# Optimization experiments

Hardware: AMD Instinct MI355X
Metric: run time of the kernel (lower is better)

## Reference

```python
import jax, jax.numpy as jnp
import numpy as np

B, S, D, H = 4, 1024, 1024, 16
HD = D // H
MAX_DIST, WIN, MAX_SPAN = 512, 256, 512
TEMP_SCALE = 0.01
EPS = 1e-5


def _ln(x, g, b):
    m = x.mean(-1, keepdims=True)
    v = ((x - m) ** 2).mean(-1, keepdims=True)
    return (x - m) * jax.lax.rsqrt(v + EPS) * g + b


def _heads(t):
    b, s, _ = t.shape
    return t.reshape(b, s, H, HD).transpose(0, 2, 1, 3)


def _merge(t):
    b, _, s, _ = t.shape
    return t.transpose(0, 2, 1, 3).reshape(b, s, D)


def _global_attn(x, Wq, bq, Wk, Wv, bv, Wo, bo):
    # MultiheadC with mask tensor passed -> is_causal=True SDPA (default 1/sqrt(HD) scale)
    q = _heads(x @ Wq.T + bq)
    k = _heads(x @ Wk.T)
    v = _heads(x @ Wv.T + bv)
    s = jnp.einsum('bhqd,bhkd->bhqk', q, k) / float(np.sqrt(HD))
    n = x.shape[1]
    causal = jnp.tril(jnp.ones((n, n), bool))
    s = jnp.where(causal, s, jnp.finfo(s.dtype).min)
    w = jax.nn.softmax(s, axis=-1)
    return _merge(jnp.einsum('bhqk,bhkd->bhqd', w, v)) @ Wo.T + bo


def _span_attn(q, k, v, temp):
    # AdaptiveSpan core: softmax(QK^T / temperature * head_dim**-0.25) V
    scale = HD ** -0.25
    qh, kh, vh = _heads(q), _heads(k), _heads(v)
    w = jax.nn.softmax(jnp.einsum('bhqd,bhkd->bhqk', qh, kh) / temp * scale, axis=-1)
    return _merge(jnp.einsum('bhqk,bhkd->bhqd', w, vh))


def _slide_win(local, span_mean, win, span_len, local_max):
    bx, sx, dx = local.shape
    temp = 1.0 + TEMP_SCALE * (1.0 - span_mean)  # sharpen=True branch
    outs = []
    for st in range(0, sx, win):  # static unrolled loop over windows (ragged slices)
        en = min(st + win, sx)
        wlen = en - st
        ks = max(0, st - span_len + win)
        ke = min(st + span_len, sx)
        klen = ke - ks
        eff = min(int(wlen * span_mean), wlen, klen, local_max)
        if eff <= 0:
            outs.append(jnp.zeros((bx, wlen, dx), local.dtype))
            continue
        o = _span_attn(local[:, st:st + eff], local[:, ks:ks + eff], local[:, ks:ks + eff], temp)
        if eff < wlen:
            o = jnp.concatenate([o, jnp.zeros((bx, wlen - eff, dx), local.dtype)], axis=1)
        outs.append(o)
    return jnp.concatenate(outs, axis=1)


def setup_inputs() -> dict:
    key = jax.random.key(0)
    ks = jax.random.split(key, 8)
    qkv_std = 1.0 / float(np.sqrt(HD))
    return {
        'x': jax.random.normal(ks[0], (B, S, D), jnp.float32),
        'ln_a_g': jnp.ones((D,), jnp.float32),
        'ln_a_b': jnp.zeros((D,), jnp.float32),
        'ln_b_g': jnp.ones((D,), jnp.float32),
        'ln_b_b': jnp.zeros((D,), jnp.float32),
        'Wq': jax.random.normal(ks[1], (D, D), jnp.float32) * qkv_std,
        'bq': jnp.zeros((D,), jnp.float32),
        'Wk': jax.random.normal(ks[2], (D, D), jnp.float32) * qkv_std,
        'Wv': jax.random.normal(ks[3], (D, D), jnp.float32) * qkv_std,
        'bv': jnp.zeros((D,), jnp.float32),
        'Wo': jax.random.normal(ks[4], (D, D), jnp.float32) * 0.02,
        'bo': jnp.zeros((D,), jnp.float32),
        'Wp': jax.random.normal(ks[5], (1, D), jnp.float32) * float(np.sqrt(2.0 / (D + 1))),
        'bp': jnp.zeros((1,), jnp.float32),
        'Wproj': jax.random.normal(ks[6], (D, 2 * D), jnp.float32) * 0.02,
        'bproj': jnp.zeros((D,), jnp.float32),
    }


def reference(x, ln_a_g, ln_a_b, ln_b_g, ln_b_b, Wq, bq, Wk, Wv, bv, Wo, bo, Wp, bp, Wproj, bproj):
    local = _ln(x, ln_a_g, ln_a_b)
    globe = _ln(x, ln_b_g, ln_b_b)
    globe_out = _global_attn(globe, Wq, bq, Wk, Wv, bv, Wo, bo)
    # Predictor: sigmoid(Linear(mean over seq))
    base_scale = jax.nn.sigmoid(globe_out.mean(axis=1) @ Wp.T + bp)  # [B, 1]
    span_scale = jnp.clip(base_scale, 0.0, 1.0)  # RL refine factor fixed at 1.0 (deterministic)
    span_mean = float(jnp.mean(span_scale))  # mirrors torch .item() host sync
    win = max(1, int(WIN * span_mean))
    span_len = max(1, int(MAX_SPAN * span_mean))
    local_max = min(MAX_DIST, span_len, win)
    local_out = _slide_win(local, span_mean, win, span_len, local_max)
    combined = jnp.concatenate([local_out, globe_out], axis=-1)
    return combined @ Wproj.T + bproj
```

## Files before the change

kernel.cpp:

```cpp
#include <hip/hip_runtime.h>
#include <math.h>

#define B_ 4
#define S_ 1024
#define D_ 1024
#define H_ 16
#define HD_ 64
#define BSD_ (B_*S_*D_)

using short8 = __attribute__((ext_vector_type(8))) short;
using f32x4  = __attribute__((ext_vector_type(4))) float;

#define MFMA16(a,b,c) __builtin_amdgcn_mfma_f32_16x16x32_bf16((a),(b),(c),0,0,0)

__device__ __forceinline__ ushort f2bf(float f) {
  uint u = __float_as_uint(f);
  return (ushort)((u + 0x7fffu + ((u >> 16) & 1u)) >> 16);
}
__device__ __forceinline__ float bf2f(ushort h) {
  return __uint_as_float(((uint)h) << 16);
}
__device__ __forceinline__ void split8(const float* p, short8* hi, short8* lo) {
  #pragma unroll
  for (int j = 0; j < 8; j++) {
    ushort h = f2bf(p[j]);
    (*hi)[j] = (short)h;
    (*lo)[j] = (short)f2bf(p[j] - bf2f(h));
  }
}
__device__ __forceinline__ void async_load16(const ushort* g, ushort* l) {
  __builtin_amdgcn_global_load_lds(
      (const __attribute__((address_space(1))) unsigned int*)g,
      (__attribute__((address_space(3))) unsigned int*)l, 16, 0, 0);
}

__device__ __forceinline__ float block_reduce_sum_256(float v, float* sbuf) {
  #pragma unroll
  for (int off = 32; off > 0; off >>= 1) v += __shfl_xor(v, off, 64);
  int lane = threadIdx.x & 63, wid = threadIdx.x >> 6;
  __syncthreads();
  if (lane == 0) sbuf[wid] = v;
  __syncthreads();
  return sbuf[0] + sbuf[1] + sbuf[2] + sbuf[3];
}

__global__ __launch_bounds__(256) void ln_kernel(const float* __restrict__ x,
                                                 const float* __restrict__ g,
                                                 const float* __restrict__ bta,
                                                 float* __restrict__ out) {
  __shared__ float sbuf[4];
  const int row = blockIdx.x;
  const float* xr = x + (size_t)row * D_;
  const int t = threadIdx.x;
  float v[4]; float s = 0.f;
  #pragma unroll
  for (int i = 0; i < 4; i++) { v[i] = xr[t + 256*i]; s += v[i]; }
  const float mean = block_reduce_sum_256(s, sbuf) * (1.0f/D_);
  float sq = 0.f;
  #pragma unroll
  for (int i = 0; i < 4; i++) { float d = v[i]-mean; sq += d*d; }
  const float var = block_reduce_sum_256(sq, sbuf) * (1.0f/D_);
  const float r = rsqrtf(var + 1e-5f);
  float* orow = out + (size_t)row * D_;
  #pragma unroll
  for (int i = 0; i < 4; i++) {
    int c = t + 256*i;
    orow[c] = (v[i]-mean)*r*g[c] + bta[c];
  }
}

__global__ __launch_bounds__(256) void ln_split_kernel(const float* __restrict__ x,
                                                       const float* __restrict__ g,
                                                       const float* __restrict__ bta,
                                                       ushort* __restrict__ out) {
  __shared__ float sbuf[4];
  const int row = blockIdx.x;
  const int t = threadIdx.x;
  const int c = t*4;
  const float* xr = x + (size_t)row * D_;
  float4 v = *(const float4*)(xr + c);
  float s = v.x + v.y + v.z + v.w;
  const float mean = block_reduce_sum_256(s, sbuf) * (1.0f/D_);
  float4 dv = make_float4(v.x-mean, v.y-mean, v.z-mean, v.w-mean);
  float sq = dv.x*dv.x + dv.y*dv.y + dv.z*dv.z + dv.w*dv.w;
  const float var = block_reduce_sum_256(sq, sbuf) * (1.0f/D_);
  const float r = rsqrtf(var + 1e-5f);
  float4 gg = *(const float4*)(g + c);
  float4 bb = *(const float4*)(bta + c);
  float n[4];
  n[0] = dv.x*r*gg.x + bb.x; n[1] = dv.y*r*gg.y + bb.y;
  n[2] = dv.z*r*gg.z + bb.z; n[3] = dv.w*r*gg.w + bb.w;
  ushort4 hi, lo;
  hi.x = f2bf(n[0]); hi.y = f2bf(n[1]); hi.z = f2bf(n[2]); hi.w = f2bf(n[3]);
  lo.x = f2bf(n[0]-bf2f(hi.x)); lo.y = f2bf(n[1]-bf2f(hi.y));
  lo.z = f2bf(n[2]-bf2f(hi.z)); lo.w = f2bf(n[3]-bf2f(hi.w));
  ushort* orow = out + (size_t)row*2048;
  *(ushort4*)(orow + c)        = hi;
  *(ushort4*)(orow + 1024 + c) = lo;
}

__global__ __launch_bounds__(256) void split_act_kernel(const float* __restrict__ in,
                                                        ushort* __restrict__ out) {
  const int idx = blockIdx.x*256 + threadIdx.x;
  const int row = idx >> 8;
  const int col4 = (idx & 255) << 2;
  const float4 a = *(const float4*)(in + (size_t)row*1024 + col4);
  ushort4 hi, lo;
  hi.x = f2bf(a.x); hi.y = f2bf(a.y); hi.z = f2bf(a.z); hi.w = f2bf(a.w);
  lo.x = f2bf(a.x - bf2f(hi.x)); lo.y = f2bf(a.y - bf2f(hi.y));
  lo.z = f2bf(a.z - bf2f(hi.z)); lo.w = f2bf(a.w - bf2f(hi.w));
  ushort* orow = out + (size_t)row*2048;
  *(ushort4*)(orow + col4)        = hi;
  *(ushort4*)(orow + 1024 + col4) = lo;
}

__global__ __launch_bounds__(256) void split_w3_kernel(const float* __restrict__ Wq,
                                                       const float* __restrict__ Wk,
                                                       const float* __restrict__ Wv,
                                                       ushort* __restrict__ out) {
  const int idx = blockIdx.x*256 + threadIdx.x;
  const int n = idx >> 8;
  const int col4 = (idx & 255) << 2;
  const float* src = (n < 1024) ? (Wq + (size_t)n*1024)
                   : (n < 2048) ? (Wk + (size_t)(n-1024)*1024)
                                : (Wv + (size_t)(n-2048)*1024);
  const float4 a = *(const float4*)(src + col4);
  ushort4 hi, lo;
  hi.x = f2bf(a.x); hi.y = f2bf(a.y); hi.z = f2bf(a.z); hi.w = f2bf(a.w);
  lo.x = f2bf(a.x - bf2f(hi.x)); lo.y = f2bf(a.y - bf2f(hi.y));
  lo.z = f2bf(a.z - bf2f(hi.z)); lo.w = f2bf(a.w - bf2f(hi.w));
  ushort* orow = out + (size_t)n*2048;
  *(ushort4*)(orow + col4)        = hi;
  *(ushort4*)(orow + 1024 + col4) = lo;
}

__global__ __launch_bounds__(256) void split_w1_kernel(const float* __restrict__ W,
                                                       ushort* __restrict__ out) {
  const int idx = blockIdx.x*256 + threadIdx.x;
  const int n = idx >> 8;
  const int col4 = (idx & 255) << 2;
  const float4 a = *(const float4*)(W + (size_t)n*1024 + col4);
  ushort4 hi, lo;
  hi.x = f2bf(a.x); hi.y = f2bf(a.y); hi.z = f2bf(a.z); hi.w = f2bf(a.w);
  lo.x = f2bf(a.x - bf2f(hi.x)); lo.y = f2bf(a.y - bf2f(hi.y));
  lo.z = f2bf(a.z - bf2f(hi.z)); lo.w = f2bf(a.w - bf2f(hi.w));
  ushort* orow = out + (size_t)n*2048;
  *(ushort4*)(orow + col4)        = hi;
  *(ushort4*)(orow + 1024 + col4) = lo;
}

__global__ __launch_bounds__(256) void cvt_bf16_kernel(const float* __restrict__ in,
                                                       ushort* __restrict__ out,
                                                       int gprshift, int ostride, int ooff) {
  const int idx = blockIdx.x*256 + threadIdx.x;
  const int row = idx >> gprshift;
  const int col4 = (idx & ((1 << gprshift) - 1)) << 2;
  const int ncols = 4 << gprshift;
  const float4 a = *(const float4*)(in + (size_t)row*ncols + col4);
  ushort4 hi;
  hi.x = f2bf(a.x); hi.y = f2bf(a.y); hi.z = f2bf(a.z); hi.w = f2bf(a.w);
  *(ushort4*)(out + (size_t)row*ostride + ooff + col4) = hi;
}

__global__ __launch_bounds__(256) void bias_cat_kernel(const float* __restrict__ bq,
                                                       const float* __restrict__ bv,
                                                       float* __restrict__ out) {
  const int n = blockIdx.x*256 + threadIdx.x;
  out[n] = (n < 1024) ? bq[n] : (n < 2048) ? 0.f : bv[n-2048];
}

__global__ __launch_bounds__(256) void mfma_gemm2(
    const ushort* __restrict__ A, const ushort* __restrict__ Bw,
    const float* __restrict__ bias, float* __restrict__ C,
    int Kh, int ldc) {
  __shared__ __align__(16) ushort Ash[128*32];
  __shared__ __align__(16) ushort Asl[128*32];
  __shared__ __align__(16) ushort Bsh[128*32];
  __shared__ __align__(16) ushort Bsl[128*32];
  const int lda = 2*Kh;
  const int tid = threadIdx.x;
  const int bm = blockIdx.y * 128, bn = blockIdx.x * 128;
  const int wave = tid >> 6, lane = tid & 63;
  const int wm = wave >> 1, wn = wave & 1;
  const int lm = lane & 15, q = lane >> 4;
  const int lrow = lane >> 2;
  const int sw = (((lane & 3) ^ (lrow & 3)) << 3);

  f32x4 acc[4][4];
  #pragma unroll
  for (int i = 0; i < 4; i++)
    #pragma unroll
    for (int j = 0; j < 4; j++)
      acc[i][j] = (f32x4){0.f,0.f,0.f,0.f};

  const ushort* Agh = A  + (size_t)(bm + wave*32 + lrow)*lda + sw;
  const ushort* Agl = Agh + Kh;
  const ushort* Bgh = Bw + (size_t)(bn + wave*32 + lrow)*lda + sw;
  const ushort* Bgl = Bgh + Kh;
  const size_t r16a = (size_t)16*lda;
  ushort* AhD0 = &Ash[(wave*32)*32];      ushort* AhD1 = &Ash[(wave*32+16)*32];
  ushort* AlD0 = &Asl[(wave*32)*32];      ushort* AlD1 = &Asl[(wave*32+16)*32];
  ushort* BhD0 = &Bsh[(wave*32)*32];      ushort* BhD1 = &Bsh[(wave*32+16)*32];
  ushort* BlD0 = &Bsl[(wave*32)*32];      ushort* BlD1 = &Bsl[(wave*32+16)*32];
  const int rsw  = ((q ^ (lm & 3)) << 3);
  const int aoff = (wm*64 + lm)*32 + rsw;
  const int boff = (wn*64 + lm)*32 + rsw;

  for (int k0 = 0; k0 < Kh; k0 += 32) {
    __syncthreads();
    async_load16(Agh + k0, AhD0);
    async_load16(Agh + r16a + k0, AhD1);
    async_load16(Agl + k0, AlD0);
    async_load16(Agl + r16a + k0, AlD1);
    async_load16(Bgh + k0, BhD0);
    async_load16(Bgh + r16a + k0, BhD1);
    async_load16(Bgl + k0, BlD0);
    async_load16(Bgl + r16a + k0, BlD1);
    __syncthreads();
    short8 ah[4], al[4], bh[4], bl[4];
    #pragma unroll
    for (int mt = 0; mt < 4; mt++) {
      ah[mt] = *(const short8*)&Ash[aoff + mt*512];
      al[mt] = *(const short8*)&Asl[aoff + mt*512];
    }
    #pragma unroll
    for (int nt = 0; nt < 4; nt++) {
      bh[nt] = *(const short8*)&Bsh[boff + nt*512];
      bl[nt] = *(const short8*)&Bsl[boff + nt*512];
    }
    #pragma unroll
    for (int mt = 0; mt < 4; mt++)
      #pragma unroll
      for (int nt = 0; nt < 4; nt++) {
        f32x4 a = acc[mt][nt];
        a = MFMA16(ah[mt], bh[nt], a);
        a = MFMA16(al[mt], bh[nt], a);
        a = MFMA16(ah[mt], bl[nt], a);
        acc[mt][nt] = a;
      }
  }

  #pragma unroll
  for (int mt = 0; mt < 4; mt++) {
    #pragma unroll
    for (int nt = 0; nt < 4; nt++) {
      const int n = bn + wn*64 + nt*16 + lm;
      const float bb = bias ? bias[n] : 0.f;
      #pragma unroll
      for (int reg = 0; reg < 4; reg++) {
        const int m = bm + wm*64 + mt*16 + q*4 + reg;
        C[(size_t)m*ldc + n] = acc[mt][nt][reg] + bb;
      }
    }
  }
}

__global__ __launch_bounds__(256) void mfma_gemm(
    const ushort* __restrict__ A, const ushort* __restrict__ Bw,
    const float* __restrict__ bias, float* __restrict__ C,
    int K, int ldc) {
  __shared__ __align__(16) ushort As[128*32];
  __shared__ __align__(16) ushort Bs[128*32];
  const int tid = threadIdx.x;
  const int bm = blockIdx.y * 128, bn = blockIdx.x * 128;
  const int wave = tid >> 6, lane = tid & 63;
  const int wm = wave >> 1, wn = wave & 1;
  const int lm = lane & 15, q = lane >> 4;
  const int lrow = lane >> 2;
  const int sw = (((lane & 3) ^ (lrow & 3)) << 3);

  f32x4 acc[4][4];
  #pragma unroll
  for (int i = 0; i < 4; i++)
    #pragma unroll
    for (int j = 0; j < 4; j++)
      acc[i][j] = (f32x4){0.f,0.f,0.f,0.f};

  const ushort* Ar0 = A  + (size_t)(bm + wave*32 + lrow)*K + sw;
  const ushort* Br0 = Bw + (size_t)(bn + wave*32 + lrow)*K + sw;
  const size_t r16 = (size_t)16*K;
  ushort* AsD0 = &As[(wave*32)*32];
  ushort* AsD1 = &As[(wave*32 + 16)*32];
  ushort* BsD0 = &Bs[(wave*32)*32];
  ushort* BsD1 = &Bs[(wave*32 + 16)*32];
  const int rsw  = ((q ^ (lm & 3)) << 3);
  const int aoff0 = (wm*64 + lm)*32 + rsw;
  const int boff0 = (wn*64 + lm)*32 + rsw;

  for (int k0 = 0; k0 < K; k0 += 32) {
    __syncthreads();
    async_load16(Ar0 + k0, AsD0);
    async_load16(Ar0 + r16 + k0, AsD1);
    async_load16(Br0 + k0, BsD0);
    async_load16(Br0 + r16 + k0, BsD1);
    __syncthreads();
    short8 af[4], bf[4];
    #pragma unroll
    for (int mt = 0; mt < 4; mt++) af[mt] = *(const short8*)&As[aoff0 + mt*512];
    #pragma unroll
    for (int nt = 0; nt < 4; nt++) bf[nt] = *(const short8*)&Bs[boff0 + nt*512];
    #pragma unroll
    for (int mt = 0; mt < 4; mt++)
      #pragma unroll
      for (int nt = 0; nt < 4; nt++)
        acc[mt][nt] = MFMA16(af[mt], bf[nt], acc[mt][nt]);
  }

  #pragma unroll
  for (int mt = 0; mt < 4; mt++) {
    #pragma unroll
    for (int nt = 0; nt < 4; nt++) {
      const int n = bn + wn*64 + nt*16 + lm;
      const float bb = bias ? bias[n] : 0.f;
      #pragma unroll
      for (int reg = 0; reg < 4; reg++) {
        const int m = bm + wm*64 + mt*16 + q*4 + reg;
        C[(size_t)m*ldc + n] = acc[mt][nt][reg] + bb;
      }
    }
  }
}

__global__ __launch_bounds__(256) void qk_split_kernel(const float* __restrict__ QKV,
                                                       ushort* __restrict__ Qsp,
                                                       ushort* __restrict__ Ksp) {
  const int row = blockIdx.x;
  const int b = row >> 10, s = row & 1023;
  const int t = threadIdx.x;
  const int h = t >> 4, c4 = (t & 15) * 4;
  const float* src = QKV + (size_t)row*3072 + h*64 + c4;
  const float4 qv = *(const float4*)src;
  const float4 kv = *(const float4*)(src + 1024);
  ushort4 qh, ql, kh, kl;
  qh.x=f2bf(qv.x); qh.y=f2bf(qv.y); qh.z=f2bf(qv.z); qh.w=f2bf(qv.w);
  ql.x=f2bf(qv.x-bf2f(qh.x)); ql.y=f2bf(qv.y-bf2f(qh.y));
  ql.z=f2bf(qv.z-bf2f(qh.z)); ql.w=f2bf(qv.w-bf2f(qh.w));
  kh.x=f2bf(kv.x); kh.y=f2bf(kv.y); kh.z=f2bf(kv.z); kh.w=f2bf(kv.w);
  kl.x=f2bf(kv.x-bf2f(kh.x)); kl.y=f2bf(kv.y-bf2f(kh.y));
  kl.z=f2bf(kv.z-bf2f(kh.z)); kl.w=f2bf(kv.w-bf2f(kh.w));
  ushort* qd = Qsp + ((size_t)(b*16 + h)*1024 + s)*128;
  ushort* kd = Ksp + ((size_t)(b*16 + h)*1024 + s)*128;
  *(ushort4*)(qd + c4)      = qh;
  *(ushort4*)(qd + 64 + c4) = ql;
  *(ushort4*)(kd + c4)      = kh;
  *(ushort4*)(kd + 64 + c4) = kl;
}

__global__ __launch_bounds__(256) void vt_split_kernel(const float* __restrict__ QKV,
                                                       ushort* __restrict__ Vth,
                                                       ushort* __restrict__ Vtl) {
  __shared__ float T[64][65];
  const int sc = blockIdx.x;
  const int bh = blockIdx.y;
  const int b = bh >> 4, h = bh & 15;
  const int t = threadIdx.x;
  {
    const int r = t >> 2, c16 = (t & 3) * 16;
    const float* src = QKV + ((size_t)(b*1024 + sc*64 + r))*3072 + 2048 + h*64 + c16;
    #pragma unroll
    for (int j = 0; j < 4; j++)
      *(float4*)&T[r][c16 + j*4] = *(const float4*)(src + j*4);
  }
  __syncthreads();
  const int d = t >> 2, s16 = (t & 3) * 16;
  short8 h0, h1, l0, l1;
  #pragma unroll
  for (int j = 0; j < 8; j++) {
    float v = T[s16 + j][d];
    ushort hh = f2bf(v);
    h0[j] = (short)hh; l0[j] = (short)f2bf(v - bf2f(hh));
  }
  #pragma unroll
  for (int j = 0; j < 8; j++) {
    float v = T[s16 + 8 + j][d];
    ushort hh = f2bf(v);
    h1[j] = (short)hh; l1[j] = (short)f2bf(v - bf2f(hh));
  }
  const size_t off = ((size_t)bh*64 + d)*1024 + sc*64 + s16;
  *(short8*)(Vth + off)     = h0;
  *(short8*)(Vth + off + 8) = h1;
  *(short8*)(Vtl + off)     = l0;
  *(short8*)(Vtl + off + 8) = l1;
}

__global__ __launch_bounds__(256) void gattn_mfma(
    const ushort* __restrict__ Qsp, const ushort* __restrict__ Ksp,
    const ushort* __restrict__ Vth, const ushort* __restrict__ Vtl,
    float* __restrict__ O) {
  __shared__ __align__(16) char su[64*136*2];
  __shared__ __align__(16) ushort Vc[64*136];
  ushort* Kc = (ushort*)su;
  float*  Pf = (float*)su;
  const int bh = blockIdx.y;
  const int b = bh >> 4, h = bh & 15;
  const int tid = threadIdx.x;
  const int w = tid >> 6, lane = tid & 63;
  const int lm = lane & 15, q = lane >> 4;
  const ushort* Qb_ = Qsp + (size_t)bh * (1024*128);
  const ushort* Kb_ = Ksp + (size_t)bh * (1024*128);
  const ushort* Vhb = Vth + (size_t)bh * (64*1024);
  const ushort* Vlb = Vtl + (size_t)bh * (64*1024);

  for (int half = 0; half < 2; ++half) {
    const int qt = half ? blockIdx.x : 15 - blockIdx.x;
    short8 qh[2], ql[2];
    {
      const ushort* qr = Qb_ + (size_t)(qt*64 + w*16 + lm)*128 + q*8;
      qh[0] = *(const short8*)(qr);
      qh[1] = *(const short8*)(qr + 32);
      ql[0] = *(const short8*)(qr + 64);
      ql[1] = *(const short8*)(qr + 96);
    }
    f32x4 of[4];
    float mst[4], lst[4];
    #pragma unroll
    for (int nt = 0; nt < 4; nt++) of[nt] = (f32x4){0.f,0.f,0.f,0.f};
    #pragma unroll
    for (int rm = 0; rm < 4; rm++) { mst[rm] = -INFINITY; lst[rm] = 0.f; }
    const int nkt = qt + 1;
    for (int kt = 0; kt < nkt; ++kt) {
      __syncthreads();
      #pragma unroll
      for (int i = 0; i < 4; i++) {
        const int slot = i*256 + tid;
        const int row = slot >> 4, c8 = slot & 15;
        *(float4*)&Kc[row*136 + c8*8] =
            *(const float4*)(Kb_ + (size_t)(kt*64 + row)*128 + c8*8);
        const ushort* vsrc = ((c8 < 8) ? Vhb : Vlb) + (size_t)row*1024 + kt*64 + (c8&7)*8;
        *(float4*)&Vc[row*136 + c8*8] = *(const float4*)vsrc;
      }
      __syncthreads();
      f32x4 sS[4];
      #pragma unroll
      for (int nt = 0; nt < 4; nt++) {
        const ushort* kr = &Kc[(nt*16 + lm)*136 + q*8];
        const short8 kh0 = *(const short8*)(kr);
        const short8 kh1 = *(const short8*)(kr + 32);
        const short8 kl0 = *(const short8*)(kr + 64);
        const short8 kl1 = *(const short8*)(kr + 96);
        f32x4 a = (f32x4){0.f,0.f,0.f,0.f};
        a = MFMA16(qh[0], kh0, a);
        a = MFMA16(ql[0], kh0, a);
        a = MFMA16(qh[0], kl0, a);
        a = MFMA16(qh[1], kh1, a);
        a = MFMA16(ql[1], kh1, a);
        a = MFMA16(qh[1], kl1, a);
        sS[nt] = a;
      }
      const int ktbase = kt*64;
      const int qrow0 = qt*64 + w*16 + q*4;
      #pragma unroll
      for (int rm = 0; rm < 4; rm++) {
        const int qrow = qrow0 + rm;
        float v[4];
        #pragma unroll
        for (int nt = 0; nt < 4; nt++) {
          const int kcol = ktbase + nt*16 + lm;
          const float x = sS[nt][rm]*0.125f;
          v[nt] = (kcol <= qrow) ? x : -INFINITY;
        }
        float tm = fmaxf(fmaxf(v[0],v[1]), fmaxf(v[2],v[3]));
        #pragma unroll
        for (int off = 1; off < 16; off <<= 1) tm = fmaxf(tm, __shfl_xor(tm, off, 64));
        const float nm = fmaxf(mst[rm], tm);
        const float alpha = __expf(mst[rm] - nm);
        float ps = 0.f;
        #pragma unroll
        for (int nt = 0; nt < 4; nt++) {
          float p = __expf(v[nt] - nm);
          sS[nt][rm] = p;
          ps += p;
        }
        #pragma unroll
        for (int off = 1; off < 16; off <<= 1) ps += __shfl_xor(ps, off, 64);
        lst[rm] = lst[rm]*alpha + ps;
        mst[rm] = nm;
        #pragma unroll
        for (int nt = 0; nt < 4; nt++) of[nt][rm] *= alpha;
      }
      __syncthreads();
      #pragma unroll
      for (int rm = 0; rm < 4; rm++)
        #pragma unroll
        for (int nt = 0; nt < 4; nt++)
          Pf[(w*16 + q*4 + rm)*66 + nt*16 + lm] = sS[nt][rm];
      __syncthreads();
      short8 ph[2], pl[2];
      {
        const float* prow = &Pf[(w*16 + lm)*66];
        float pv[16];
        *(float4*)&pv[0]  = *(const float4*)(prow + q*8);
        *(float4*)&pv[4]  = *(const float4*)(prow + q*8 + 4);
        *(float4*)&pv[8]  = *(const float4*)(prow + 32 + q*8);
        *(float4*)&pv[12] = *(const float4*)(prow + 32 + q*8 + 4);
        split8(&pv[0], &ph[0], &pl[0]);
        split8(&pv[8], &ph[1], &pl[1]);
      }
      #pragma unroll
      for (int nt = 0; nt < 4; nt++) {
        const ushort* vr = &Vc[(nt*16 + lm)*136 + q*8];
        const short8 vh0 = *(const short8*)(vr);
        const short8 vh1 = *(const short8*)(vr + 32);
        const short8 vl0 = *(const short8*)(vr + 64);
        const short8 vl1 = *(const short8*)(vr + 96);
        f32x4 a = of[nt];
        a = MFMA16(ph[0], vh0, a);
        a = MFMA16(pl[0], vh0, a);
        a = MFMA16(ph[0], vl0, a);
        a = MFMA16(ph[1], vh1, a);
        a = MFMA16(pl[1], vh1, a);
        a = MFMA16(ph[1], vl1, a);
        of[nt] = a;
      }
    }
    #pragma unroll
    for (int rm = 0; rm < 4; rm++) {
      const float inv = 1.0f / lst[rm];
      const int s = qt*64 + w*16 + q*4 + rm;
      float* orow = O + ((size_t)(b*1024 + s))*1024 + h*64;
      #pragma unroll
      for (int nt = 0; nt < 4; nt++)
        orow[nt*16 + lm] = of[nt][rm] * inv;
    }
  }
}

__global__ __launch_bounds__(256) void seqmean1_kernel(const float* __restrict__ g,
                                                       float* __restrict__ part) {
  const int d = blockIdx.x*256 + threadIdx.x;
  const int sc = blockIdx.y;
  const int b = blockIdx.z;
  const float* p = g + ((size_t)b*S_ + sc*128)*D_ + d;
  float s = 0.f;
  #pragma unroll 4
  for (int i = 0; i < 128; i++) s += p[(size_t)i*D_];
  part[((size_t)(b*8 + sc))*D_ + d] = s;
}
__global__ __launch_bounds__(256) void seqmean2_kernel(const float* __restrict__ part,
                                                       float* __restrict__ mbd) {
  const int d = blockIdx.x*256 + threadIdx.x;
  const int b = blockIdx.y;
  float s = 0.f;
  #pragma unroll
  for (int i = 0; i < 8; i++) s += part[((size_t)(b*8 + i))*D_ + d];
  mbd[b*D_ + d] = s * (1.0f/S_);
}

__global__ __launch_bounds__(256) void predictor_kernel(
    const float* __restrict__ mbd, const float* __restrict__ Wp,
    const float* __restrict__ bp, float* __restrict__ fpar, int* __restrict__ ipar) {
  __shared__ float sbuf[4];
  __shared__ float sdots[4];
  const int tid = threadIdx.x;
  for (int b = 0; b < 4; b++) {
    float psum = 0.f;
    for (int d = tid; d < D_; d += 256) psum += mbd[b*D_ + d]*Wp[d];
    float tot = block_reduce_sum_256(psum, sbuf);
    if (tid == 0) sdots[b] = tot;
  }
  __syncthreads();
  if (tid == 0) {
    float smv = 0.f;
    for (int b = 0; b < 4; b++) {
      float z = sdots[b] + bp[0];
      smv += 1.0f/(1.0f + expf(-z));
    }
    smv *= 0.25f;
    int win = max(1, (int)(256.0f*smv));
    int span_len = max(1, (int)(512.0f*smv));
    int local_max = min(512, min(span_len, win));
    float temp = 1.0f + 0.01f*(1.0f - smv);
    int n_win = (S_ + win - 1)/win;
    fpar[0] = smv; fpar[1] = temp;
    ipar[0] = win; ipar[1] = span_len; ipar[2] = local_max; ipar[3] = n_win;
  }
}

#define LDP 68
__global__ __launch_bounds__(256) void lattn_kernel(
    const float* __restrict__ Lc, ushort* __restrict__ Out,
    const int* __restrict__ ip, const float* __restrict__ fpp) {
  __shared__ __align__(16) float Qs[HD_][LDP];
  __shared__ __align__(16) float KPs[64][LDP];
  __shared__ __align__(16) float Vs[64][LDP];
  const int n_win = ip[3];
  const int win = ip[0], span_len = ip[1], local_max = ip[2];
  const float sm = fpp[0], temp = fpp[1];
  const int bh = blockIdx.y;
  const int b = bh >> 4, h = bh & 15;
  const int tid = threadIdx.x;
  const int tx = tid & 15, ty = tid >> 4;
  const float sc = 0.35355339059327373f / temp;
  for (int w = blockIdx.x; w < n_win; w += gridDim.x) {
    const int st = w * win;
    const int en = min(st + win, S_); const int wlen = en - st;
    const int ks = max(0, st - span_len + win);
    const int ke = min(st + span_len, S_); const int klen = ke - ks;
    int eff = (int)((double)wlen * (double)sm);
    eff = min(min(eff, wlen), min(klen, local_max));
    if (eff <= 0) continue;
    const int nt = (eff + 63) >> 6;
    for (int qt = 0; qt < nt; ++qt) {
      const int qn = min(64, eff - qt*64);
      __syncthreads();
      #pragma unroll
      for (int c = 0; c < 4; c++) {
        int f = tid + c*256;
        int r = f >> 4;
        int dc = (f & 15) << 2;
        float4 q4 = make_float4(0.f,0.f,0.f,0.f);
        if (r < qn) q4 = *(const float4*)(Lc + ((size_t)(b*S_ + st + qt*64 + r)) * D_ + h*HD_ + dc);
        Qs[dc+0][r]=q4.x; Qs[dc+1][r]=q4.y; Qs[dc+2][r]=q4.z; Qs[dc+3][r]=q4.w;
      }
      float o[4][4] = {{0.f,0.f,0.f,0.f},{0.f,0.f,0.f,0.f},{0.f,0.f,0.f,0.f},{0.f,0.f,0.f,0.f}};
      float mrow[4], lrow[4];
      #pragma unroll
      for (int i=0;i<4;i++){ mrow[i] = -INFINITY; lrow[i] = 0.f; }
      for (int kt = 0; kt < nt; ++kt) {
        const int kn = min(64, eff - kt*64);
        __syncthreads();
        #pragma unroll
        for (int c = 0; c < 4; c++) {
          int f = tid + c*256;
          int r = f >> 4;
          int dc = (f & 15) << 2;
          float4 k4 = make_float4(0.f,0.f,0.f,0.f);
          if (r < kn) k4 = *(const float4*)(Lc + ((size_t)(b*S_ + ks + kt*64 + r)) * D_ + h*HD_ + dc);
          KPs[dc+0][r]=k4.x; KPs[dc+1][r]=k4.y; KPs[dc+2][r]=k4.z; KPs[dc+3][r]=k4.w;
          *(float4*)&Vs[r][dc] = k4;
        }
        __syncthreads();
        float s[4][4] = {{0.f,0.f,0.f,0.f},{0.f,0.f,0.f,0.f},{0.f,0.f,0.f,0.f},{0.f,0.f,0.f,0.f}};
        #pragma unroll 8
        for (int d = 0; d < HD_; ++d) {
          const float4 a  = *(const float4*)&Qs[d][ty*4];
          const float4 bb = *(const float4*)&KPs[d][tx*4];
          const float av[4]={a.x,a.y,a.z,a.w};
          const float bv[4]={bb.x,bb.y,bb.z,bb.w};
          #pragma unroll
          for (int i=0;i<4;i++)
            #pragma unroll
            for (int j=0;j<4;j++)
              s[i][j] += av[i]*bv[j];
        }
        #pragma unroll
        for (int i=0;i<4;i++) {
          #pragma unroll
          for (int j=0;j<4;j++) {
            float lg = s[i][j]*sc;
            if (kt*64 + tx*4 + j >= eff) lg = -INFINITY;
            s[i][j] = lg;
          }
        }
        #pragma unroll
        for (int i=0;i<4;i++) {
          float tm = fmaxf(fmaxf(s[i][0],s[i][1]), fmaxf(s[i][2],s[i][3]));
          #pragma unroll
          for (int off=1; off<16; off<<=1) tm = fmaxf(tm, __shfl_xor(tm, off, 64));
          const float nm = fmaxf(mrow[i], tm);
          const float alpha = __expf(mrow[i]-nm);
          float ps = 0.f;
          #pragma unroll
          for (int j=0;j<4;j++){ float p = __expf(s[i][j]-nm); s[i][j]=p; ps += p; }
          #pragma unroll
          for (int off=1; off<16; off<<=1) ps += __shfl_xor(ps, off, 64);
          lrow[i] = lrow[i]*alpha + ps;
          mrow[i] = nm;
          #pragma unroll
          for (int j=0;j<4;j++) o[i][j] *= alpha;
        }
        __syncthreads();
        #pragma unroll
        for (int i=0;i<4;i++)
          #pragma unroll
          for (int j=0;j<4;j++)
            KPs[tx*4+j][ty*4+i] = s[i][j];
        __syncthreads();
        #pragma unroll 8
        for (int kk = 0; kk < 64; ++kk) {
          const float4 a  = *(const float4*)&KPs[kk][ty*4];
          const float4 bb = *(const float4*)&Vs[kk][tx*4];
          const float av[4]={a.x,a.y,a.z,a.w};
          const float bv[4]={bb.x,bb.y,bb.z,bb.w};
          #pragma unroll
          for (int i=0;i<4;i++)
            #pragma unroll
            for (int j=0;j<4;j++)
              o[i][j] += av[i]*bv[j];
        }
      }
      #pragma unroll
      for (int i=0;i<4;i++){
        const int r = ty*4 + i;
        if (r < qn) {
          const float inv = 1.0f / lrow[i];
          ushort4 ov;
          ov.x = f2bf(o[i][0]*inv); ov.y = f2bf(o[i][1]*inv);
          ov.z = f2bf(o[i][2]*inv); ov.w = f2bf(o[i][3]*inv);
          *(ushort4*)(Out + ((size_t)(b*S_ + st + qt*64 + r)) * 2048 + h*HD_ + tx*4) = ov;
        }
      }
    }
  }
}

extern "C" void kernel_launch(void* const* d_in, const int* in_sizes, int n_in,
                              void* d_out, int out_size, void* d_ws, size_t ws_size,
                              hipStream_t stream) {
  const float* x      = (const float*)d_in[0];
  const float* ln_a_g = (const float*)d_in[1];
  const float* ln_a_b = (const float*)d_in[2];
  const float* ln_b_g = (const float*)d_in[3];
  const float* ln_b_b = (const float*)d_in[4];
  const float* Wq     = (const float*)d_in[5];
  const float* bq     = (const float*)d_in[6];
  const float* Wk     = (const float*)d_in[7];
  const float* Wv     = (const float*)d_in[8];
  const float* bv     = (const float*)d_in[9];
  const float* Wo     = (const float*)d_in[10];
  const float* bo     = (const float*)d_in[11];
  const float* Wp     = (const float*)d_in[12];
  const float* bp     = (const float*)d_in[13];
  const float* Wproj  = (const float*)d_in[14];
  const float* bproj  = (const float*)d_in[15];
  float* out = (float*)d_out;
  float* ws  = (float*)d_ws;

  float* QKVf = ws;
  float* buf0 = ws + 12582912;
  float* glo  = ws + 16777216;
  float* loc  = ws + 20971520;
  float* biascat = ws + 25165824;
  float* mbd  = biascat + 4096;
  float* fpar = mbd + 4096;
  int*   ipar = (int*)(fpar + 8);
  ushort* Acat  = (ushort*)(ws + 25182208);
  ushort* Bqkv  = Acat + 12582912;
  ushort* Bo    = Bqkv + 9437184;
  ushort* Qsp = Acat;
  ushort* Ksp = Bqkv;
  ushort* Vth = (ushort*)loc;
  ushort* Vtl = Vth + 4194304;
  float*  part = (float*)Acat;
  ushort* A3  = (ushort*)ws;
  ushort* B3  = A3 + 8388608;

  const dim3 blk(256);

  ln_split_kernel<<<dim3(B_*S_), blk, 0, stream>>>(x, ln_b_g, ln_b_b, Acat);
  split_w3_kernel<<<dim3(3072), blk, 0, stream>>>(Wq, Wk, Wv, Bqkv);
  bias_cat_kernel<<<dim3(12), blk, 0, stream>>>(bq, bv, biascat);
  mfma_gemm2<<<dim3(24, 32), blk, 0, stream>>>(Acat, Bqkv, biascat, QKVf, 1024, 3072);
  qk_split_kernel<<<dim3(4096), blk, 0, stream>>>(QKVf, Qsp, Ksp);
  vt_split_kernel<<<dim3(16, 64), blk, 0, stream>>>(QKVf, Vth, Vtl);
  gattn_mfma<<<dim3(8, 64), blk, 0, stream>>>(Qsp, Ksp, Vth, Vtl, buf0);
  split_act_kernel<<<dim3(4096), blk, 0, stream>>>(buf0, Acat);
  split_w1_kernel<<<dim3(1024), blk, 0, stream>>>(Wo, Bo);
  mfma_gemm2<<<dim3(8, 32), blk, 0, stream>>>(Acat, Bo, bo, glo, 1024, 1024);
  seqmean1_kernel<<<dim3(4, 8, B_), blk, 0, stream>>>(glo, part);
  seqmean2_kernel<<<dim3(4, B_), blk, 0, stream>>>(part, mbd);
  predictor_kernel<<<dim3(1), blk, 0, stream>>>(mbd, Wp, bp, fpar, ipar);
  ln_kernel<<<dim3(B_*S_), blk, 0, stream>>>(x, ln_a_g, ln_a_b, loc);
  hipMemsetAsync(A3, 0, (size_t)4096*2048*2, stream);
  lattn_kernel<<<dim3(64, B_*H_), blk, 0, stream>>>(loc, A3, ipar, fpar);
  cvt_bf16_kernel<<<dim3(4096), blk, 0, stream>>>(glo, A3, 8, 2048, 1024);
  cvt_bf16_kernel<<<dim3(2048), blk, 0, stream>>>(Wproj, B3, 9, 2048, 0);
  mfma_gemm<<<dim3(8, 32), blk, 0, stream>>>(A3, B3, bproj, out, 2048, 1024);
}
```

Baseline: 489.5 us.

## Fuse QKV split/transpose into GEMM epilogue and remove intermediate passes

The QKV GEMM now writes bf16 hi/lo split Q and K directly in head layout, and writes V transposed through shared memory, replacing the fp32 QKV buffer and two follow-up split kernels. The Wo GEMM epilogue also writes the bf16 copy of its output into the final concat buffer, removing a conversion kernel. The bias concat is folded into the weight split kernel. The memset is replaced by explicit zero writes in the local attention kernel. In the attention kernel, Pf gets its own shared buffer so two barriers can be dropped, at the cost of more shared memory. Workspace aliasing is reorganised so the fused outputs do not overwrite buffers that are still in use.

New measurement: 483.6 us. No clear change (-1.2%).

```diff
diff --git a/kernel.cpp b/kernel.cpp
--- a/kernel.cpp
+++ b/kernel.cpp
@@ -117,7 +117,10 @@
 __global__ __launch_bounds__(256) void split_w3_kernel(const float* __restrict__ Wq,
                                                        const float* __restrict__ Wk,
                                                        const float* __restrict__ Wv,
-                                                       ushort* __restrict__ out) {
+                                                       const float* __restrict__ bq,
+                                                       const float* __restrict__ bv,
+                                                       ushort* __restrict__ out,
+                                                       float* __restrict__ biascat) {
   const int idx = blockIdx.x*256 + threadIdx.x;
   const int n = idx >> 8;
   const int col4 = (idx & 255) << 2;
@@ -132,6 +135,8 @@
   ushort* orow = out + (size_t)n*2048;
   *(ushort4*)(orow + col4)        = hi;
   *(ushort4*)(orow + 1024 + col4) = lo;
+  if (idx < 3072)
+    biascat[idx] = (idx < 1024) ? bq[idx] : (idx < 2048) ? 0.f : bv[idx-2048];
 }
 
 __global__ __launch_bounds__(256) void split_w1_kernel(const float* __restrict__ W,
@@ -162,17 +167,142 @@
   *(ushort4*)(out + (size_t)row*ostride + ooff + col4) = hi;
 }
 
-__global__ __launch_bounds__(256) void bias_cat_kernel(const float* __restrict__ bq,
-                                                       const float* __restrict__ bv,
-                                                       float* __restrict__ out) {
-  const int n = blockIdx.x*256 + threadIdx.x;
-  out[n] = (n < 1024) ? bq[n] : (n < 2048) ? 0.f : bv[n-2048];
+__global__ __launch_bounds__(256) void mfma_gemm_qkv(
+    const ushort* __restrict__ A, const ushort* __restrict__ Bw,
+    const float* __restrict__ bias,
+    ushort* __restrict__ Qsp, ushort* __restrict__ Ksp,
+    ushort* __restrict__ Vth, ushort* __restrict__ Vtl, int Kh) {
+  __shared__ __align__(16) ushort smem[17408];
+  ushort* Ash = smem;
+  ushort* Asl = smem + 4096;
+  ushort* Bsh = smem + 8192;
+  ushort* Bsl = smem + 12288;
+  const int lda = 2*Kh;
+  const int tid = threadIdx.x;
+  const int bm = blockIdx.y * 128, bn = blockIdx.x * 128;
+  const int wave = tid >> 6, lane = tid & 63;
+  const int wm = wave >> 1, wn = wave & 1;
+  const int lm = lane & 15, q = lane >> 4;
+  const int lrow = lane >> 2;
+  const int sw = (((lane & 3) ^ (lrow & 3)) << 3);
+
+  f32x4 acc[4][4];
+  #pragma unroll
+  for (int i = 0; i < 4; i++)
+    #pragma unroll
+    for (int j = 0; j < 4; j++)
+      acc[i][j] = (f32x4){0.f,0.f,0.f,0.f};
+
+  const ushort* Agh = A  + (size_t)(bm + wave*32 + lrow)*lda + sw;
+  const ushort* Agl = Agh + Kh;
+  const ushort* Bgh = Bw + (size_t)(bn + wave*32 + lrow)*lda + sw;
+  const ushort* Bgl = Bgh + Kh;
+  const size_t r16a = (size_t)16*lda;
+  ushort* AhD0 = &Ash[(wave*32)*32];      ushort* AhD1 = &Ash[(wave*32+16)*32];
+  ushort* AlD0 = &Asl[(wave*32)*32];      ushort* AlD1 = &Asl[(wave*32+16)*32];
+  ushort* BhD0 = &Bsh[(wave*32)*32];      ushort* BhD1 = &Bsh[(wave*32+16)*32];
+  ushort* BlD0 = &Bsl[(wave*32)*32];      ushort* BlD1 = &Bsl[(wave*32+16)*32];
+  const int rsw  = ((q ^ (lm & 3)) << 3);
+  const int aoff = (wm*64 + lm)*32 + rsw;
+  const int boff = (wn*64 + lm)*32 + rsw;
+
+  for (int k0 = 0; k0 < Kh; k0 += 32) {
+    __syncthreads();
+    async_load16(Agh + k0, AhD0);
+    async_load16(Agh + r16a + k0, AhD1);
+    async_load16(Agl + k0, AlD0);
+    async_load16(Agl + r16a + k0, AlD1);
+    async_load16(Bgh + k0, BhD0);
+    async_load16(Bgh + r16a + k0, BhD1);
+    async_load16(Bgl + k0, BlD0);
+    async_load16(Bgl + r16a + k0, BlD1);
+    __syncthreads();
+    short8 ah[4], al[4], bh[4], bl[4];
+    #pragma unroll
+    for (int mt = 0; mt < 4; mt++) {
+      ah[mt] = *(const short8*)&Ash[aoff + mt*512];
+      al[mt] = *(const short8*)&Asl[aoff + mt*512];
+    }
+    #pragma unroll
+    for (int nt = 0; nt < 4; nt++) {
+      bh[nt] = *(const short8*)&Bsh[boff + nt*512];
+      bl[nt] = *(const short8*)&Bsl[boff + nt*512];
+    }
+    #pragma unroll
+    for (int mt = 0; mt < 4; mt++)
+      #pragma unroll
+      for (int nt = 0; nt < 4; nt++) {
+        f32x4 a = acc[mt][nt];
+        a = MFMA16(ah[mt], bh[nt], a);
+        a = MFMA16(al[mt], bh[nt], a);
+        a = MFMA16(ah[mt], bl[nt], a);
+        acc[mt][nt] = a;
+      }
+  }
+
+  const int b = bm >> 10, s0 = bm & 1023;
+  if (blockIdx.x < 16) {
+    ushort* dst = (blockIdx.x < 8) ? Qsp : Ksp;
+    const int h = ((bn + wn*64) >> 6) & 15;
+    #pragma unroll
+    for (int mt = 0; mt < 4; mt++) {
+      #pragma unroll
+      for (int nt = 0; nt < 4; nt++) {
+        const int n = bn + wn*64 + nt*16 + lm;
+        const int d = nt*16 + lm;
+        const float bb = bias[n];
+        #pragma unroll
+        for (int reg = 0; reg < 4; reg++) {
+          const int s = s0 + wm*64 + mt*16 + q*4 + reg;
+          const float val = acc[mt][nt][reg] + bb;
+          const ushort hi = f2bf(val);
+          const ushort lo = f2bf(val - bf2f(hi));
+          ushort* rp = dst + ((size_t)((b*16 + h)*1024 + s))*128;
+          rp[d] = hi; rp[64 + d] = lo;
+        }
+      }
+    }
+  } else {
+    ushort* Th = smem;
+    ushort* Tl = smem + 8704;
+    #pragma unroll
+    for (int c = 0; c < 2; c++) {
+      __syncthreads();
+      if (wn == c) {
+        #pragma unroll
+        for (int mt = 0; mt < 4; mt++)
+          #pragma unroll
+          for (int nt = 0; nt < 4; nt++) {
+            const int nl = nt*16 + lm;
+            const float bb = bias[bn + c*64 + nl];
+            #pragma unroll
+            for (int reg = 0; reg < 4; reg++) {
+              const int sl = wm*64 + mt*16 + q*4 + reg;
+              const float val = acc[mt][nt][reg] + bb;
+              const ushort hi = f2bf(val);
+              const ushort lo = f2bf(val - bf2f(hi));
+              Th[nl*136 + sl] = hi;
+              Tl[nl*136 + sl] = lo;
+            }
+          }
+      }
+      __syncthreads();
+      const int nl = tid >> 2, s32 = (tid & 3)*32;
+      const int h = ((bn - 2048 + c*64) >> 6) & 15;
+      const size_t drow = ((size_t)((b*16 + h)*64 + nl))*1024 + s0 + s32;
+      #pragma unroll
+      for (int j = 0; j < 4; j++) {
+        *(short8*)(Vth + drow + j*8) = *(const short8*)&Th[nl*136 + s32 + j*8];
+        *(short8*)(Vtl + drow + j*8) = *(const short8*)&Tl[nl*136 + s32 + j*8];
+      }
+    }
+  }
 }
 
 __global__ __launch_bounds__(256) void mfma_gemm2(
     const ushort* __restrict__ A, const ushort* __restrict__ Bw,
     const float* __restrict__ bias, float* __restrict__ C,
-    int Kh, int ldc) {
+    int Kh, int ldc, ushort* __restrict__ aux) {
   __shared__ __align__(16) ushort Ash[128*32];
   __shared__ __align__(16) ushort Asl[128*32];
   __shared__ __align__(16) ushort Bsh[128*32];
@@ -249,7 +379,9 @@
       #pragma unroll
       for (int reg = 0; reg < 4; reg++) {
         const int m = bm + wm*64 + mt*16 + q*4 + reg;
-        C[(size_t)m*ldc + n] = acc[mt][nt][reg] + bb;
+        const float val = acc[mt][nt][reg] + bb;
+        C[(size_t)m*ldc + n] = val;
+        if (aux) aux[(size_t)m*2048 + 1024 + n] = f2bf(val);
       }
     }
   }
@@ -321,76 +453,13 @@
   }
 }
 
-__global__ __launch_bounds__(256) void qk_split_kernel(const float* __restrict__ QKV,
-                                                       ushort* __restrict__ Qsp,
-                                                       ushort* __restrict__ Ksp) {
-  const int row = blockIdx.x;
-  const int b = row >> 10, s = row & 1023;
-  const int t = threadIdx.x;
-  const int h = t >> 4, c4 = (t & 15) * 4;
-  const float* src = QKV + (size_t)row*3072 + h*64 + c4;
-  const float4 qv = *(const float4*)src;
-  const float4 kv = *(const float4*)(src + 1024);
-  ushort4 qh, ql, kh, kl;
-  qh.x=f2bf(qv.x); qh.y=f2bf(qv.y); qh.z=f2bf(qv.z); qh.w=f2bf(qv.w);
-  ql.x=f2bf(qv.x-bf2f(qh.x)); ql.y=f2bf(qv.y-bf2f(qh.y));
-  ql.z=f2bf(qv.z-bf2f(qh.z)); ql.w=f2bf(qv.w-bf2f(qh.w));
-  kh.x=f2bf(kv.x); kh.y=f2bf(kv.y); kh.z=f2bf(kv.z); kh.w=f2bf(kv.w);
-  kl.x=f2bf(kv.x-bf2f(kh.x)); kl.y=f2bf(kv.y-bf2f(kh.y));
-  kl.z=f2bf(kv.z-bf2f(kh.z)); kl.w=f2bf(kv.w-bf2f(kh.w));
-  ushort* qd = Qsp + ((size_t)(b*16 + h)*1024 + s)*128;
-  ushort* kd = Ksp + ((size_t)(b*16 + h)*1024 + s)*128;
-  *(ushort4*)(qd + c4)      = qh;
-  *(ushort4*)(qd + 64 + c4) = ql;
-  *(ushort4*)(kd + c4)      = kh;
-  *(ushort4*)(kd + 64 + c4) = kl;
-}
-
-__global__ __launch_bounds__(256) void vt_split_kernel(const float* __restrict__ QKV,
-                                                       ushort* __restrict__ Vth,
-                                                       ushort* __restrict__ Vtl) {
-  __shared__ float T[64][65];
-  const int sc = blockIdx.x;
-  const int bh = blockIdx.y;
-  const int b = bh >> 4, h = bh & 15;
-  const int t = threadIdx.x;
-  {
-    const int r = t >> 2, c16 = (t & 3) * 16;
-    const float* src = QKV + ((size_t)(b*1024 + sc*64 + r))*3072 + 2048 + h*64 + c16;
-    #pragma unroll
-    for (int j = 0; j < 4; j++)
-      *(float4*)&T[r][c16 + j*4] = *(const float4*)(src + j*4);
-  }
-  __syncthreads();
-  const int d = t >> 2, s16 = (t & 3) * 16;
-  short8 h0, h1, l0, l1;
-  #pragma unroll
-  for (int j = 0; j < 8; j++) {
-    float v = T[s16 + j][d];
-    ushort hh = f2bf(v);
-    h0[j] = (short)hh; l0[j] = (short)f2bf(v - bf2f(hh));
-  }
-  #pragma unroll
-  for (int j = 0; j < 8; j++) {
-    float v = T[s16 + 8 + j][d];
-    ushort hh = f2bf(v);
-    h1[j] = (short)hh; l1[j] = (short)f2bf(v - bf2f(hh));
-  }
-  const size_t off = ((size_t)bh*64 + d)*1024 + sc*64 + s16;
-  *(short8*)(Vth + off)     = h0;
-  *(short8*)(Vth + off + 8) = h1;
-  *(short8*)(Vtl + off)     = l0;
-  *(short8*)(Vtl + off + 8) = l1;
-}
-
 __global__ __launch_bounds__(256) void gattn_mfma(
     const ushort* __restrict__ Qsp, const ushort* __restrict__ Ksp,
     const ushort* __restrict__ Vth, const ushort* __restrict__ Vtl,
     float* __restrict__ O) {
-  __shared__ __align__(16) char su[64*136*2];
+  __shared__ __align__(16) ushort Kc[64*136];
   __shared__ __align__(16) ushort Vc[64*136];
-  ushort* Kc = (ushort*)su;
-  float*  Pf = (float*)su;
+  __shared__ __align__(16) float  Pf[64*66];
   const int bh = blockIdx.y;
   const int b = bh >> 4, h = bh & 15;
   const int tid = threadIdx.x;
@@ -478,13 +547,11 @@
         #pragma unroll
         for (int nt = 0; nt < 4; nt++) of[nt][rm] *= alpha;
       }
-      __syncthreads();
       #pragma unroll
       for (int rm = 0; rm < 4; rm++)
         #pragma unroll
         for (int nt = 0; nt < 4; nt++)
           Pf[(w*16 + q*4 + rm)*66 + nt*16 + lm] = sS[nt][rm];
-      __syncthreads();
       short8 ph[2], pl[2];
       {
         const float* prow = &Pf[(w*16 + lm)*66];
@@ -598,109 +665,113 @@
     const int ke = min(st + span_len, S_); const int klen = ke - ks;
     int eff = (int)((double)wlen * (double)sm);
     eff = min(min(eff, wlen), min(klen, local_max));
-    if (eff <= 0) continue;
-    const int nt = (eff + 63) >> 6;
-    for (int qt = 0; qt < nt; ++qt) {
-      const int qn = min(64, eff - qt*64);
-      __syncthreads();
-      #pragma unroll
-      for (int c = 0; c < 4; c++) {
-        int f = tid + c*256;
-        int r = f >> 4;
-        int dc = (f & 15) << 2;
-        float4 q4 = make_float4(0.f,0.f,0.f,0.f);
-        if (r < qn) q4 = *(const float4*)(Lc + ((size_t)(b*S_ + st + qt*64 + r)) * D_ + h*HD_ + dc);
-        Qs[dc+0][r]=q4.x; Qs[dc+1][r]=q4.y; Qs[dc+2][r]=q4.z; Qs[dc+3][r]=q4.w;
-      }
-      float o[4][4] = {{0.f,0.f,0.f,0.f},{0.f,0.f,0.f,0.f},{0.f,0.f,0.f,0.f},{0.f,0.f,0.f,0.f}};
-      float mrow[4], lrow[4];
-      #pragma unroll
-      for (int i=0;i<4;i++){ mrow[i] = -INFINITY; lrow[i] = 0.f; }
-      for (int kt = 0; kt < nt; ++kt) {
-        const int kn = min(64, eff - kt*64);
+    if (eff > 0) {
+      const int nt = (eff + 63) >> 6;
+      for (int qt = 0; qt < nt; ++qt) {
+        const int qn = min(64, eff - qt*64);
         __syncthreads();
         #pragma unroll
         for (int c = 0; c < 4; c++) {
           int f = tid + c*256;
           int r = f >> 4;
           int dc = (f & 15) << 2;
-          float4 k4 = make_float4(0.f,0.f,0.f,0.f);
-          if (r < kn) k4 = *(const float4*)(Lc + ((size_t)(b*S_ + ks + kt*64 + r)) * D_ + h*HD_ + dc);
-          KPs[dc+0][r]=k4.x; KPs[dc+1][r]=k4.y; KPs[dc+2][r]=k4.z; KPs[dc+3][r]=k4.w;
-          *(float4*)&Vs[r][dc] = k4;
+          float4 q4 = make_float4(0.f,0.f,0.f,0.f);
+          if (r < qn) q4 = *(const float4*)(Lc + ((size_t)(b*S_ + st + qt*64 + r)) * D_ + h*HD_ + dc);
+          Qs[dc+0][r]=q4.x; Qs[dc+1][r]=q4.y; Qs[dc+2][r]=q4.z; Qs[dc+3][r]=q4.w;
         }
-        __syncthreads();
-        float s[4][4] = {{0.f,0.f,0.f,0.f},{0.f,0.f,0.f,0.f},{0.f,0.f,0.f,0.f},{0.f,0.f,0.f,0.f}};
-        #pragma unroll 8
-        for (int d = 0; d < HD_; ++d) {
-          const float4 a  = *(const float4*)&Qs[d][ty*4];
-          const float4 bb = *(const float4*)&KPs[d][tx*4];
-          const float av[4]={a.x,a.y,a.z,a.w};
-          const float bv[4]={bb.x,bb.y,bb.z,bb.w};
+        float o[4][4] = {{0.f,0.f,0.f,0.f},{0.f,0.f,0.f,0.f},{0.f,0.f,0.f,0.f},{0.f,0.f,0.f,0.f}};
+        float mrow[4], lrow[4];
+        #pragma unroll
+        for (int i=0;i<4;i++){ mrow[i] = -INFINITY; lrow[i] = 0.f; }
+        for (int kt = 0; kt < nt; ++kt) {
+          const int kn = min(64, eff - kt*64);
+          __syncthreads();
+          #pragma unroll
+          for (int c = 0; c < 4; c++) {
+            int f = tid + c*256;
+            int r = f >> 4;
+            int dc = (f & 15) << 2;
+            float4 k4 = make_float4(0.f,0.f,0.f,0.f);
+            if (r < kn) k4 = *(const float4*)(Lc + ((size_t)(b*S_ + ks + kt*64 + r)) * D_ + h*HD_ + dc);
+            KPs[dc+0][r]=k4.x; KPs[dc+1][r]=k4.y; KPs[dc+2][r]=k4.z; KPs[dc+3][r]=k4.w;
+            *(float4*)&Vs[r][dc] = k4;
+          }
+          __syncthreads();
+          float s[4][4] = {{0.f,0.f,0.f,0.f},{0.f,0.f,0.f,0.f},{0.f,0.f,0.f,0.f},{0.f,0.f,0.f,0.f}};
+          #pragma unroll 8
+          for (int d = 0; d < HD_; ++d) {
+            const float4 a  = *(const float4*)&Qs[d][ty*4];
+            const float4 bb = *(const float4*)&KPs[d][tx*4];
+            const float av[4]={a.x,a.y,a.z,a.w};
+            const float bv[4]={bb.x,bb.y,bb.z,bb.w};
+            #pragma unroll
+            for (int i=0;i<4;i++)
+              #pragma unroll
+              for (int j=0;j<4;j++)
+                s[i][j] += av[i]*bv[j];
+          }
+          #pragma unroll
+          for (int i=0;i<4;i++) {
+            #pragma unroll
+            for (int j=0;j<4;j++) {
+              float lg = s[i][j]*sc;
+              if (kt*64 + tx*4 + j >= eff) lg = -INFINITY;
+              s[i][j] = lg;
+            }
+          }
+          #pragma unroll
+          for (int i=0;i<4;i++) {
+            float tm = fmaxf(fmaxf(s[i][0],s[i][1]), fmaxf(s[i][2],s[i][3]));
+            #pragma unroll
+            for (int off=1; off<16; off<<=1) tm = fmaxf(tm, __shfl_xor(tm, off, 64));
+            const float nm = fmaxf(mrow[i], tm);
+            const float alpha = __expf(mrow[i]-nm);
+            float ps = 0.f;
+            #pragma unroll
+            for (int j=0;j<4;j++){ float p = __expf(s[i][j]-nm); s[i][j]=p; ps += p; }
+            #pragma unroll
+            for (int off=1; off<16; off<<=1) ps += __shfl_xor(ps, off, 64);
+            lrow[i] = lrow[i]*alpha + ps;
+            mrow[i] = nm;
+            #pragma unroll
+            for (int j=0;j<4;j++) o[i][j] *= alpha;
+          }
+          __syncthreads();
           #pragma unroll
           for (int i=0;i<4;i++)
             #pragma unroll
             for (int j=0;j<4;j++)
-              s[i][j] += av[i]*bv[j];
-        }
-        #pragma unroll
-        for (int i=0;i<4;i++) {
-          #pragma unroll
-          for (int j=0;j<4;j++) {
-            float lg = s[i][j]*sc;
-            if (kt*64 + tx*4 + j >= eff) lg = -INFINITY;
-            s[i][j] = lg;
+              KPs[tx*4+j][ty*4+i] = s[i][j];
+          __syncthreads();
+          #pragma unroll 8
+          for (int kk = 0; kk < 64; ++kk) {
+            const float4 a  = *(const float4*)&KPs[kk][ty*4];
+            const float4 bb = *(const float4*)&Vs[kk][tx*4];
+            const float av[4]={a.x,a.y,a.z,a.w};
+            const float bv[4]={bb.x,bb.y,bb.z,bb.w};
+            #pragma unroll
+            for (int i=0;i<4;i++)
+              #pragma unroll
+              for (int j=0;j<4;j++)
+                o[i][j] += av[i]*bv[j];
           }
         }
         #pragma unroll
-        for (int i=0;i<4;i++) {
-          float tm = fmaxf(fmaxf(s[i][0],s[i][1]), fmaxf(s[i][2],s[i][3]));
-          #pragma unroll
-          for (int off=1; off<16; off<<=1) tm = fmaxf(tm, __shfl_xor(tm, off, 64));
-          const float nm = fmaxf(mrow[i], tm);
-          const float alpha = __expf(mrow[i]-nm);
-          float ps = 0.f;
-          #pragma unroll
-          for (int j=0;j<4;j++){ float p = __expf(s[i][j]-nm); s[i][j]=p; ps += p; }
-          #pragma unroll
-          for (int off=1; off<16; off<<=1) ps += __shfl_xor(ps, off, 64);
-          lrow[i] = lrow[i]*alpha + ps;
-          mrow[i] = nm;
-          #pragma unroll
-          for (int j=0;j<4;j++) o[i][j] *= alpha;
+        for (int i=0;i<4;i++){
+          const int r = ty*4 + i;
+          if (r < qn) {
+            const float inv = 1.0f / lrow[i];
+            ushort4 ov;
+            ov.x = f2bf(o[i][0]*inv); ov.y = f2bf(o[i][1]*inv);
+            ov.z = f2bf(o[i][2]*inv); ov.w = f2bf(o[i][3]*inv);
+            *(ushort4*)(Out + ((size_t)(b*S_ + st + qt*64 + r)) * 2048 + h*HD_ + tx*4) = ov;
+          }
         }
-        __syncthreads();
-        #pragma unroll
-        for (int i=0;i<4;i++)
-          #pragma unroll
-          for (int j=0;j<4;j++)
-            KPs[tx*4+j][ty*4+i] = s[i][j];
-        __syncthreads();
-        #pragma unroll 8
-        for (int kk = 0; kk < 64; ++kk) {
-          const float4 a  = *(const float4*)&KPs[kk][ty*4];
-          const float4 bb = *(const float4*)&Vs[kk][tx*4];
-          const float av[4]={a.x,a.y,a.z,a.w};
-          const float bv[4]={bb.x,bb.y,bb.z,bb.w};
-          #pragma unroll
-          for (int i=0;i<4;i++)
-            #pragma unroll
-            for (int j=0;j<4;j++)
-              o[i][j] += av[i]*bv[j];
-        }
-      }
-      #pragma unroll
-      for (int i=0;i<4;i++){
-        const int r = ty*4 + i;
-        if (r < qn) {
-          const float inv = 1.0f / lrow[i];
-          ushort4 ov;
-          ov.x = f2bf(o[i][0]*inv); ov.y = f2bf(o[i][1]*inv);
-          ov.z = f2bf(o[i][2]*inv); ov.w = f2bf(o[i][3]*inv);
-          *(ushort4*)(Out + ((size_t)(b*S_ + st + qt*64 + r)) * 2048 + h*HD_ + tx*4) = ov;
-        }
-      }
-    }
+      }
+    }
+    const ushort4 z = {0,0,0,0};
+    for (int r = max(eff, 0) + ty; r < wlen; r += 16)
+      *(ushort4*)(Out + ((size_t)(b*S_ + st + r)) * 2048 + h*HD_ + tx*4) = z;
   }
 }
 
@@ -725,8 +796,12 @@
   const float* bproj  = (const float*)d_in[15];
   float* out = (float*)d_out;
   float* ws  = (float*)d_ws;
-
-  float* QKVf = ws;
+  ushort* wsu = (ushort*)d_ws;
+
+  ushort* Qsp = wsu;
+  ushort* Ksp = wsu + 8388608;
+  ushort* Vth = wsu + 16777216;
+  ushort* Vtl = wsu + 20971520;
   float* buf0 = ws + 12582912;
   float* glo  = ws + 16777216;
   float* loc  = ws + 20971520;
@@ -737,33 +812,25 @@
   ushort* Acat  = (ushort*)(ws + 25182208);
   ushort* Bqkv  = Acat + 12582912;
   ushort* Bo    = Bqkv + 9437184;
-  ushort* Qsp = Acat;
-  ushort* Ksp = Bqkv;
-  ushort* Vth = (ushort*)loc;
-  ushort* Vtl = Vth + 4194304;
   float*  part = (float*)Acat;
-  ushort* A3  = (ushort*)ws;
-  ushort* B3  = A3 + 8388608;
+  ushort* A3  = wsu;
+  ushort* B3  = wsu + 8388608;
 
   const dim3 blk(256);
 
   ln_split_kernel<<<dim3(B_*S_), blk, 0, stream>>>(x, ln_b_g, ln_b_b, Acat);
-  split_w3_kernel<<<dim3(3072), blk, 0, stream>>>(Wq, Wk, Wv, Bqkv);
-  bias_cat_kernel<<<dim3(12), blk, 0, stream>>>(bq, bv, biascat);
-  mfma_gemm2<<<dim3(24, 32), blk, 0, stream>>>(Acat, Bqkv, biascat, QKVf, 1024, 3072);
-  qk_split_kernel<<<dim3(4096), blk, 0, stream>>>(QKVf, Qsp, Ksp);
-  vt_split_kernel<<<dim3(16, 64), blk, 0, stream>>>(QKVf, Vth, Vtl);
+  split_w3_kernel<<<dim3(3072), blk, 0, stream>>>(Wq, Wk, Wv, bq, bv, Bqkv, biascat);
+  mfma_gemm_qkv<<<dim3(24, 32), blk, 0, stream>>>(Acat, Bqkv, biascat,
+                                                  Qsp, Ksp, Vth, Vtl, 1024);
   gattn_mfma<<<dim3(8, 64), blk, 0, stream>>>(Qsp, Ksp, Vth, Vtl, buf0);
   split_act_kernel<<<dim3(4096), blk, 0, stream>>>(buf0, Acat);
   split_w1_kernel<<<dim3(1024), blk, 0, stream>>>(Wo, Bo);
-  mfma_gemm2<<<dim3(8, 32), blk, 0, stream>>>(Acat, Bo, bo, glo, 1024, 1024);
+  mfma_gemm2<<<dim3(8, 32), blk, 0, stream>>>(Acat, Bo, bo, glo, 1024, 1024, A3);
   seqmean1_kernel<<<dim3(4, 8, B_), blk, 0, stream>>>(glo, part);
   seqmean2_kernel<<<dim3(4, B_), blk, 0, stream>>>(part, mbd);
   predictor_kernel<<<dim3(1), blk, 0, stream>>>(mbd, Wp, bp, fpar, ipar);
   ln_kernel<<<dim3(B_*S_), blk, 0, stream>>>(x, ln_a_g, ln_a_b, loc);
-  hipMemsetAsync(A3, 0, (size_t)4096*2048*2, stream);
   lattn_kernel<<<dim3(64, B_*H_), blk, 0, stream>>>(loc, A3, ipar, fpar);
-  cvt_bf16_kernel<<<dim3(4096), blk, 0, stream>>>(glo, A3, 8, 2048, 1024);
   cvt_bf16_kernel<<<dim3(2048), blk, 0, stream>>>(Wproj, B3, 9, 2048, 0);
   mfma_gemm<<<dim3(8, 32), blk, 0, stream>>>(A3, B3, bproj, out, 2048, 1024);
 }
```
